# Kernel optimization log

Measured on AMD Instinct MI355X. Metric: run time of the kernel, lower is better.

The kernel has to match this reference:

```python
import math
import jax
import jax.numpy as jnp
import numpy as np
from jax import lax

B, IC, OC, K, STYLE_DIM, H, W = 16, 512, 512, 3, 512, 32, 32
EPS = 1e-8


def _blur_kernel():
    # make_kernel([1,3,3,1]) outer product, normalized, times upsample_factor**2 (=4)
    k = jnp.array([1.0, 3.0, 3.0, 1.0], dtype=jnp.float32)
    k2 = k[None, :] * k[:, None]
    k2 = k2 / k2.sum()
    return k2 * 4.0  # [4,4]


def setup_inputs() -> dict:
    key = jax.random.key(0)
    k1, k2, k3, k4 = jax.random.split(key, 4)
    return {
        "input": jax.random.normal(k1, (B, IC, H, W), dtype=jnp.float32),
        "style": jax.random.normal(k2, (B, STYLE_DIM), dtype=jnp.float32),
        "weight": jax.random.normal(k3, (1, OC, IC, K, K), dtype=jnp.float32),
        "mod_weight": jax.random.normal(k4, (IC, STYLE_DIM), dtype=jnp.float32),
        "mod_bias": jnp.ones((IC,), dtype=jnp.float32),  # bias_init=1
    }


def reference(input, style, weight, mod_weight, mod_bias):
    batch, in_ch, h, w_sp = input.shape
    out_ch, ksz = weight.shape[1], weight.shape[3]

    # EqualLinear modulation: scale = 1/sqrt(style_dim), lr_mul=1, no activation
    mod_scale = 1.0 / math.sqrt(mod_weight.shape[1])
    s = style @ (mod_weight * mod_scale).T + mod_bias  # [B, IC]

    # modulate + demodulate
    conv_scale = 1.0 / math.sqrt(in_ch * ksz * ksz)
    wmod = conv_scale * weight * s[:, None, :, None, None]  # [B, OC, IC, K, K]
    demod = lax.rsqrt(jnp.sum(wmod * wmod, axis=(2, 3, 4)) + EPS)  # [B, OC]
    wmod = wmod * demod[:, :, None, None, None]

    # conv_transpose2d(stride=2, padding=0, groups=batch) == per-sample conv with
    # lhs_dilation=2, full padding (K-1), spatially flipped kernel in OIHW layout.
    w_conv = wmod[:, :, :, ::-1, ::-1]  # [B, OC, IC, K, K]

    def one_sample(x, wk):
        # x: [IC, H, W], wk: [OC, IC, K, K] -> [OC, 2H+K-2+1, ...] (65x65 here)
        return lax.conv_general_dilated(
            x[None], wk, window_strides=(1, 1),
            padding=[(ksz - 1, ksz - 1)] * 2,
            lhs_dilation=(2, 2),
            dimension_numbers=("NCHW", "OIHW", "NCHW"))[0]

    out = jax.vmap(one_sample)(input, w_conv)  # [B, OC, 65, 65]

    # Blur: upfirdn2d(up=1, down=1, pad=(1,1)) with symmetric 4x4 kernel -> depthwise conv
    bk = _blur_kernel()
    out = jnp.pad(out, ((0, 0), (0, 0), (1, 1), (1, 1)))
    dk = jnp.tile(bk[None, None], (out_ch, 1, 1, 1))  # [OC, 1, 4, 4]
    out = lax.conv_general_dilated(
        out, dk, window_strides=(1, 1), padding="VALID",
        feature_group_count=out_ch,
        dimension_numbers=("NCHW", "OIHW", "NCHW"))  # [B, OC, 64, 64]
    return out
```

## Files before the change

### kernel.cpp

```cpp
#include <hip/hip_runtime.h>
#include <stdint.h>

typedef unsigned int uint32;
typedef unsigned short u16;
typedef short short8 __attribute__((ext_vector_type(8)));
typedef float floatx4 __attribute__((ext_vector_type(4)));

#define OFF_S      0u
#define OFF_DS     32768u
#define OFF_WSUM   65536u
#define OFF_WPACK  1114112u
#define OFF_XST    5832704u
#define OFF_U      22609920u

__device__ __forceinline__ u16 f2bf(float x){
    uint32 u = __float_as_uint(x);
    uint32 r = (u + 0x7FFFu + ((u>>16)&1u)) >> 16;
    return (u16)r;
}
__device__ __forceinline__ float bf2f(u16 h){
    return __uint_as_float(((uint32)h)<<16);
}

#define GLL16(gp, lp) \
    __builtin_amdgcn_global_load_lds( \
        (const __attribute__((address_space(1))) void*)(gp), \
        (__attribute__((address_space(3))) void*)(lp), 16, 0, 0)

__global__ __launch_bounds__(256) void k_style(const float* __restrict__ style,
                                               const float* __restrict__ mw,
                                               const float* __restrict__ mb,
                                               float* __restrict__ s){
    int gid = blockIdx.x*4 + (threadIdx.x>>6);
    int lane = threadIdx.x & 63;
    int b = gid>>9, ic = gid & 511;
    const float* sp = style + b*512;
    const float* wp = mw + (size_t)ic*512;
    float acc = 0.f;
    for (int d=lane; d<512; d+=64) acc += sp[d]*wp[d];
    for (int off=32; off; off>>=1) acc += __shfl_down(acc, off, 64);
    if (lane==0) s[b*512+ic] = acc*0.044194173824159216f + mb[ic];
}

__global__ __launch_bounds__(256) void k_wprep(const float* __restrict__ w,
                                               float* __restrict__ wsum,
                                               u16* __restrict__ wp){
    int idx = blockIdx.x*256 + threadIdx.x;
    const float* p = w + (size_t)idx*9;
    float vv[9]; float a = 0.f;
    #pragma unroll
    for (int t=0;t<9;++t){ float v=p[t]; vv[t]=v; a += v*v; }
    wsum[idx] = a;
    #pragma unroll
    for (int t=0;t<9;++t) wp[(size_t)t*262144 + idx] = f2bf(vv[t]);
}

__global__ __launch_bounds__(256) void k_dscale(const float* __restrict__ s,
                                                const float* __restrict__ wsum,
                                                float* __restrict__ ds){
    int gid = blockIdx.x*4 + (threadIdx.x>>6);
    int lane = threadIdx.x & 63;
    int b = gid>>9, oc = gid & 511;
    const float* sp = s + b*512;
    const float* wp = wsum + (size_t)oc*512;
    float acc=0.f;
    for (int d=lane; d<512; d+=64){ float sv = sp[d]; acc += sv*sv*wp[d]; }
    for (int off=32; off; off>>=1) acc += __shfl_down(acc, off, 64);
    if (lane==0){
        const float cs = 0.014731391274719738f;
        ds[b*512+oc] = cs * rsqrtf(cs*cs*acc + 1e-8f);
    }
}

__global__ __launch_bounds__(256) void k_xst(const float* __restrict__ in,
                                             const float* __restrict__ s,
                                             u16* __restrict__ xst){
    int bx = blockIdx.x;
    int b = bx>>5, i = bx&31;
    __shared__ u16 tr[32*520];
    int tid = threadIdx.x;
    int j = tid & 31;
    for (int ic = tid>>5; ic < 512; ic += 8){
        float v = in[((size_t)(b*512+ic)*32 + i)*32 + j] * s[b*512+ic];
        tr[j*520 + ic] = f2bf(v);
    }
    __syncthreads();
    for (int v = tid; v < 2048; v += 256){
        int jj = v>>6, ic8 = (v&63)*8;
        *(uint4*)(xst + (size_t)(b*1024 + i*32 + jj)*512 + ic8) =
            *(const uint4*)(&tr[jj*520 + ic8]);
    }
}

__global__ __launch_bounds__(256) void k_gemm(const u16* __restrict__ A,
                                              const u16* __restrict__ Bx,
                                              u16* __restrict__ C,
                                              int Ncols){
    int n0 = blockIdx.x * 128;
    int m0 = blockIdx.y * 128;
    int tid = threadIdx.x, lane = tid & 63, w = tid >> 6;
    int wm = w>>1, wn = w&1;
    int np = lane & 15, qq = lane >> 4;

    __shared__ __align__(16) u16 Asm[128*64];
    __shared__ __align__(16) u16 Bsm[128*64];

    int rsub = lane >> 3;
    int gsw  = (lane & 7) ^ rsub;

    floatx4 acc[4][4] = {};

    for (int k0 = 0; k0 < 512; k0 += 64){
        #pragma unroll
        for (int q = 0; q < 4; ++q){
            int row = q*32 + w*8 + rsub;
            GLL16(A + (size_t)(m0+row)*512 + k0 + gsw*8, &Asm[(q*32 + w*8)*64]);
        }
        #pragma unroll
        for (int q = 0; q < 4; ++q){
            int row = q*32 + w*8 + rsub;
            GLL16(Bx + (size_t)(n0+row)*512 + k0 + gsw*8, &Bsm[(q*32 + w*8)*64]);
        }
        __syncthreads();
        #pragma unroll
        for (int kk = 0; kk < 2; ++kk){
            short8 af[4], bf[4];
            #pragma unroll
            for (int mf = 0; mf < 4; ++mf){
                int row = wm*64 + mf*16 + np;
                int gs = (kk*4 + qq) ^ (np & 7);
                af[mf] = *(const short8*)(&Asm[row*64 + gs*8]);
            }
            #pragma unroll
            for (int nf = 0; nf < 4; ++nf){
                int row = wn*64 + nf*16 + np;
                int gs = (kk*4 + qq) ^ (np & 7);
                bf[nf] = *(const short8*)(&Bsm[row*64 + gs*8]);
            }
            #pragma unroll
            for (int mf = 0; mf < 4; ++mf)
                #pragma unroll
                for (int nf = 0; nf < 4; ++nf)
                    acc[mf][nf] = __builtin_amdgcn_mfma_f32_16x16x32_bf16(
                        af[mf], bf[nf], acc[mf][nf], 0,0,0);
        }
        __syncthreads();
    }
    #pragma unroll
    for (int mf = 0; mf < 4; ++mf){
        #pragma unroll
        for (int reg = 0; reg < 4; ++reg){
            int m = m0 + wm*64 + mf*16 + qq*4 + reg;
            size_t base = (size_t)m * Ncols;
            #pragma unroll
            for (int nf = 0; nf < 4; ++nf){
                int n = n0 + wn*64 + nf*16 + np;
                C[base + n] = f2bf(acc[mf][nf][reg]);
            }
        }
    }
}

__global__ __launch_bounds__(256) void k_blur2(const u16* __restrict__ U,
                                               const float* __restrict__ ds,
                                               float* __restrict__ out,
                                               int b0, int Ncols){
    int oc = blockIdx.x;
    int bp = blockIdx.y;
    int b  = b0 + bp;
    __shared__ __align__(16) char ubuf[18432];
    __shared__ __align__(16) float tsm[65*66];
    u16*  Usm = (u16*)ubuf;
    float* hsm = (float*)ubuf;
    int tid = threadIdx.x;

    const u16* src0 = U + (size_t)oc*Ncols + (size_t)bp*1024;
    size_t tapstride = (size_t)512 * Ncols;
    for (int i = tid; i < 1152; i += 256){
        int tap = i>>7, c8 = i & 127;
        *(uint4*)(&Usm[tap*1024 + c8*8]) = *(const uint4*)(src0 + tap*tapstride + c8*8);
    }
    __syncthreads();

    for (int idx = tid; idx < 4225; idx += 256){
        float v = 0.f;
        if (idx < 1089){
            int Y = idx/33, X = idx - Y*33;
            #pragma unroll
            for (int da = 0; da < 2; ++da){
                int iy = Y - da;
                if ((unsigned)iy < 32u){
                    #pragma unroll
                    for (int db = 0; db < 2; ++db){
                        int jx = X - db;
                        if ((unsigned)jx < 32u)
                            v += bf2f(Usm[(6*da + 2*db)*1024 + iy*32 + jx]);
                    }
                }
            }
            tsm[(2*Y)*66 + 2*X] = v;
        } else if (idx < 2145){
            int loc = idx - 1089, Y = loc>>5, X = loc & 31;
            #pragma unroll
            for (int da = 0; da < 2; ++da){
                int iy = Y - da;
                if ((unsigned)iy < 32u)
                    v += bf2f(Usm[(6*da + 1)*1024 + iy*32 + X]);
            }
            tsm[(2*Y)*66 + 2*X + 1] = v;
        } else if (idx < 3201){
            int loc = idx - 2145, Y = loc/33, X = loc - Y*33;
            #pragma unroll
            for (int db = 0; db < 2; ++db){
                int jx = X - db;
                if ((unsigned)jx < 32u)
                    v += bf2f(Usm[(3 + 2*db)*1024 + Y*32 + jx]);
            }
            tsm[(2*Y+1)*66 + 2*X] = v;
        } else {
            int loc = idx - 3201, Y = loc>>5, X = loc & 31;
            v = bf2f(Usm[4*1024 + Y*32 + X]);
            tsm[(2*Y+1)*66 + 2*X + 1] = v;
        }
    }
    __syncthreads();

    for (int idx = tid; idx < 4160; idx += 256){
        int y = idx>>6, X = idx & 63;
        const float* trow = tsm + y*66;
        float v = 3.f*trow[X] + 3.f*trow[X+1];
        if (X > 0)  v += trow[X-1];
        if (X < 63) v += trow[X+2];
        hsm[y*64 + X] = v;
    }
    __syncthreads();

    float dsc = ds[b*512 + oc] * (1.f/16.f);
    float* op = out + (size_t)(b*512 + oc) * 4096;
    for (int idx = tid; idx < 4096; idx += 256){
        int Y = idx>>6, X = idx & 63;
        float v = 3.f*hsm[Y*64 + X] + 3.f*hsm[(Y+1)*64 + X];
        if (Y > 0)  v += hsm[(Y-1)*64 + X];
        if (Y < 63) v += hsm[(Y+2)*64 + X];
        op[idx] = dsc * v;
    }
}

extern "C" void kernel_launch(void* const* d_in, const int* in_sizes, int n_in,
                              void* d_out, int out_size, void* d_ws, size_t ws_size,
                              hipStream_t stream){
    const float* input  = (const float*)d_in[0];
    const float* style  = (const float*)d_in[1];
    const float* weight = (const float*)d_in[2];
    const float* mw     = (const float*)d_in[3];
    const float* mb     = (const float*)d_in[4];
    float* out = (float*)d_out;
    char* ws = (char*)d_ws;
    float* s     = (float*)(ws + OFF_S);
    float* ds    = (float*)(ws + OFF_DS);
    float* wsum  = (float*)(ws + OFF_WSUM);
    u16*   wpack = (u16*)(ws + OFF_WPACK);
    u16*   xst   = (u16*)(ws + OFF_XST);
    u16*   U     = (u16*)(ws + OFF_U);

    int NB;
    if      (ws_size >= (size_t)OFF_U + (size_t)4608*16384*2) NB = 16;
    else if (ws_size >= (size_t)OFF_U + (size_t)4608*8192*2)  NB = 8;
    else                                                       NB = 4;
    int npass = 16 / NB;
    int Ncols = NB * 1024;

    k_style <<<2048, 256, 0, stream>>>(style, mw, mb, s);
    k_wprep <<<1024, 256, 0, stream>>>(weight, wsum, wpack);
    k_dscale<<<2048, 256, 0, stream>>>(s, wsum, ds);
    k_xst   <<<512,  256, 0, stream>>>(input, s, xst);

    for (int p = 0; p < npass; ++p){
        const u16* xp = xst + (size_t)p * NB * 1024 * 512;
        k_gemm <<<dim3(Ncols/128, 36), 256, 0, stream>>>(wpack, xp, U, Ncols);
        k_blur2<<<dim3(512, NB),       256, 0, stream>>>(U, ds, out, p*NB, Ncols);
    }
}
```

Baseline: 357.1 us.

## Stage GEMM epilogue through LDS and fold blur into polyphase tap sums

The GEMM epilogue now writes bf16 results into a swizzled shared-memory tile and stores them to global memory as 16-byte vectors, replacing the scattered 2-byte stores. The blur kernel is restructured: the transposed-conv scatter and horizontal blur are folded into polyphase row sums computed directly from the nine tap planes. These sums are packed as bf16 pairs, and a vertical pass then writes float4 outputs. This removes the large float staging buffer and several passes, at the cost of an extra bf16 rounding on the intermediate horizontal sums.

```diff
diff --git a/kernel.cpp b/kernel.cpp
--- a/kernel.cpp
+++ b/kernel.cpp
@@ -102,8 +102,10 @@
     int wm = w>>1, wn = w&1;
     int np = lane & 15, qq = lane >> 4;
 
-    __shared__ __align__(16) u16 Asm[128*64];
-    __shared__ __align__(16) u16 Bsm[128*64];
+    __shared__ __align__(16) char smem[32768];
+    u16* Asm = (u16*)smem;
+    u16* Bsm = (u16*)(smem + 16384);
+    u16* Csm = (u16*)smem;
 
     int rsub = lane >> 3;
     int gsw  = (lane & 7) ^ rsub;
@@ -124,7 +126,7 @@
         __syncthreads();
         #pragma unroll
         for (int kk = 0; kk < 2; ++kk){
-            short8 af[4], bf[4];
+            short8 af[4], bfr[4];
             #pragma unroll
             for (int mf = 0; mf < 4; ++mf){
                 int row = wm*64 + mf*16 + np;
@@ -135,14 +137,14 @@
             for (int nf = 0; nf < 4; ++nf){
                 int row = wn*64 + nf*16 + np;
                 int gs = (kk*4 + qq) ^ (np & 7);
-                bf[nf] = *(const short8*)(&Bsm[row*64 + gs*8]);
+                bfr[nf] = *(const short8*)(&Bsm[row*64 + gs*8]);
             }
             #pragma unroll
             for (int mf = 0; mf < 4; ++mf)
                 #pragma unroll
                 for (int nf = 0; nf < 4; ++nf)
                     acc[mf][nf] = __builtin_amdgcn_mfma_f32_16x16x32_bf16(
-                        af[mf], bf[nf], acc[mf][nf], 0,0,0);
+                        af[mf], bfr[nf], acc[mf][nf], 0,0,0);
         }
         __syncthreads();
     }
@@ -150,13 +152,24 @@
     for (int mf = 0; mf < 4; ++mf){
         #pragma unroll
         for (int reg = 0; reg < 4; ++reg){
-            int m = m0 + wm*64 + mf*16 + qq*4 + reg;
-            size_t base = (size_t)m * Ncols;
+            int row = wm*64 + mf*16 + qq*4 + reg;
             #pragma unroll
             for (int nf = 0; nf < 4; ++nf){
-                int n = n0 + wn*64 + nf*16 + np;
-                C[base + n] = f2bf(acc[mf][nf][reg]);
+                int col = wn*64 + nf*16 + np;
+                int c = col >> 3;
+                Csm[row*128 + ((c ^ (row & 15)) << 3) + (col & 7)] =
+                    f2bf(acc[mf][nf][reg]);
             }
+        }
+    }
+    __syncthreads();
+    {
+        int c = tid & 15;
+        #pragma unroll
+        for (int it = 0; it < 8; ++it){
+            int row = it*16 + (tid >> 4);
+            uint4 v = *(const uint4*)(&Csm[row*128 + ((c ^ (row & 15)) << 3)]);
+            *(uint4*)(C + (size_t)(m0+row)*Ncols + n0 + c*8) = v;
         }
     }
 }
@@ -168,81 +181,78 @@
     int oc = blockIdx.x;
     int bp = blockIdx.y;
     int b  = b0 + bp;
-    __shared__ __align__(16) char ubuf[18432];
-    __shared__ __align__(16) float tsm[65*66];
-    u16*  Usm = (u16*)ubuf;
-    float* hsm = (float*)ubuf;
+    __shared__ __align__(16) u16 Usm[9*1024];
+    __shared__ __align__(16) u16 HRsm[3*32*64];
     int tid = threadIdx.x;
 
     const u16* src0 = U + (size_t)oc*Ncols + (size_t)bp*1024;
     size_t tapstride = (size_t)512 * Ncols;
-    for (int i = tid; i < 1152; i += 256){
-        int tap = i>>7, c8 = i & 127;
-        *(uint4*)(&Usm[tap*1024 + c8*8]) = *(const uint4*)(src0 + tap*tapstride + c8*8);
-    }
-    __syncthreads();
-
-    for (int idx = tid; idx < 4225; idx += 256){
-        float v = 0.f;
-        if (idx < 1089){
-            int Y = idx/33, X = idx - Y*33;
-            #pragma unroll
-            for (int da = 0; da < 2; ++da){
-                int iy = Y - da;
-                if ((unsigned)iy < 32u){
-                    #pragma unroll
-                    for (int db = 0; db < 2; ++db){
-                        int jx = X - db;
-                        if ((unsigned)jx < 32u)
-                            v += bf2f(Usm[(6*da + 2*db)*1024 + iy*32 + jx]);
-                    }
-                }
-            }
-            tsm[(2*Y)*66 + 2*X] = v;
-        } else if (idx < 2145){
-            int loc = idx - 1089, Y = loc>>5, X = loc & 31;
-            #pragma unroll
-            for (int da = 0; da < 2; ++da){
-                int iy = Y - da;
-                if ((unsigned)iy < 32u)
-                    v += bf2f(Usm[(6*da + 1)*1024 + iy*32 + X]);
-            }
-            tsm[(2*Y)*66 + 2*X + 1] = v;
-        } else if (idx < 3201){
-            int loc = idx - 2145, Y = loc/33, X = loc - Y*33;
-            #pragma unroll
-            for (int db = 0; db < 2; ++db){
-                int jx = X - db;
-                if ((unsigned)jx < 32u)
-                    v += bf2f(Usm[(3 + 2*db)*1024 + Y*32 + jx]);
-            }
-            tsm[(2*Y+1)*66 + 2*X] = v;
-        } else {
-            int loc = idx - 3201, Y = loc>>5, X = loc & 31;
-            v = bf2f(Usm[4*1024 + Y*32 + X]);
-            tsm[(2*Y+1)*66 + 2*X + 1] = v;
-        }
-    }
-    __syncthreads();
-
-    for (int idx = tid; idx < 4160; idx += 256){
-        int y = idx>>6, X = idx & 63;
-        const float* trow = tsm + y*66;
-        float v = 3.f*trow[X] + 3.f*trow[X+1];
-        if (X > 0)  v += trow[X-1];
-        if (X < 63) v += trow[X+2];
-        hsm[y*64 + X] = v;
+    #pragma unroll
+    for (int it = 0; it < 5; ++it){
+        int i = tid + it*256;
+        if (i < 1152){
+            int tap = i>>7, c8 = i & 127;
+            *(uint4*)(&Usm[tap*1024 + c8*8]) =
+                *(const uint4*)(src0 + tap*tapstride + c8*8);
+        }
+    }
+    __syncthreads();
+
+    #pragma unroll
+    for (int it = 0; it < 12; ++it){
+        int task = tid + it*256;
+        int a = task >> 10, rem = task & 1023;
+        int i = rem >> 5, u = rem & 31;
+        const u16* base = Usm + a*3072 + i*32;
+        float u0  = bf2f(base[u]);
+        float u1  = bf2f(base[1024 + u]);
+        float u2  = bf2f(base[2048 + u]);
+        float u0p = (u < 31) ? bf2f(base[u + 1])        : 0.f;
+        float u1m = (u > 0)  ? bf2f(base[1024 + u - 1]) : 0.f;
+        float u1p = (u < 31) ? bf2f(base[1024 + u + 1]) : 0.f;
+        float u2m = (u > 0)  ? bf2f(base[2048 + u - 1]) : 0.f;
+        float HRe = u1m + 3.f*(u0 + u2m + u1) + u0p + u2;
+        float HRo = u0 + u2m + 3.f*(u1 + u0p + u2) + u1p;
+        uint32 packed = (uint32)f2bf(HRe) | ((uint32)f2bf(HRo) << 16);
+        *(uint32*)(&HRsm[(a*32 + i)*64 + 2*u]) = packed;
     }
     __syncthreads();
 
     float dsc = ds[b*512 + oc] * (1.f/16.f);
     float* op = out + (size_t)(b*512 + oc) * 4096;
-    for (int idx = tid; idx < 4096; idx += 256){
-        int Y = idx>>6, X = idx & 63;
-        float v = 3.f*hsm[Y*64 + X] + 3.f*hsm[(Y+1)*64 + X];
-        if (Y > 0)  v += hsm[(Y-1)*64 + X];
-        if (Y < 63) v += hsm[(Y+2)*64 + X];
-        op[idx] = dsc * v;
+    #pragma unroll
+    for (int it = 0; it < 4; ++it){
+        int task = tid + it*256;
+        int Y = task >> 4, X0 = (task & 15) * 4;
+        float o0=0.f,o1=0.f,o2=0.f,o3=0.f;
+        int v = Y >> 1;
+        #define ACCROW(aa, ii, ww) do{ \
+            int _i = (ii); \
+            if ((unsigned)_i < 32u){ \
+                uint2 rv = *(const uint2*)(&HRsm[((aa)*32 + _i)*64 + X0]); \
+                o0 += (ww)*__uint_as_float((rv.x & 0xffffu) << 16); \
+                o1 += (ww)*__uint_as_float(rv.x & 0xffff0000u); \
+                o2 += (ww)*__uint_as_float((rv.y & 0xffffu) << 16); \
+                o3 += (ww)*__uint_as_float(rv.y & 0xffff0000u); \
+            } }while(0)
+        if ((Y & 1) == 0){
+            ACCROW(1, v-1, 1.f);
+            ACCROW(0, v,   3.f);
+            ACCROW(2, v-1, 3.f);
+            ACCROW(1, v,   3.f);
+            ACCROW(0, v+1, 1.f);
+            ACCROW(2, v,   1.f);
+        } else {
+            ACCROW(0, v,   1.f);
+            ACCROW(2, v-1, 1.f);
+            ACCROW(1, v,   3.f);
+            ACCROW(0, v+1, 3.f);
+            ACCROW(2, v,   3.f);
+            ACCROW(1, v+1, 1.f);
+        }
+        #undef ACCROW
+        float4 res = make_float4(dsc*o0, dsc*o1, dsc*o2, dsc*o3);
+        *(float4*)(op + Y*64 + X0) = res;
     }
 }
 
```

Result: faster. 338.3 us (-5.3%).
